# Optimization experiments

Measured on AMD Instinct MI355X. Metric: run time of the kernel, lower is better.

Reference implementation:

```python
import jax, jax.numpy as jnp
import numpy as np
from jax import lax

MAX_ALPHA = 0.00015
MAX_BETA = 0.00015
NOISE_GRAIN = 0.05
LN_EPS = 1e-5


def gaussian_blur(x, ksize, sigma):
    # depthwise 2D gaussian blur, same padding; x: [B, C, H, W]
    r = ksize // 2
    g = jnp.exp(-(jnp.linspace(-r, r, ksize, dtype=x.dtype) ** 2) / (2.0 * sigma ** 2))
    g = g / g.sum()
    k2d = g[:, None] * g[None, :]                       # [k, k]
    C = x.shape[1]
    kernel = jnp.broadcast_to(k2d, (C, 1, ksize, ksize))  # OIHW, depthwise
    return lax.conv_general_dilated(
        x, kernel, window_strides=(1, 1), padding=[(r, r), (r, r)],
        feature_group_count=C, dimension_numbers=('NCHW', 'OIHW', 'NCHW'))


def setup_inputs() -> dict:
    key = jax.random.key(0)
    ks = jax.random.split(key, 8)
    B, C, H, W = 8, 3, 1024, 1024
    L, D = 1024, 512
    Dh = D // 4
    return {
        'x_bg': jax.random.uniform(ks[0], (B, C, H, W), dtype=jnp.float32),
        'bottleneck_feat': jax.random.normal(ks[1], (B, L, D), dtype=jnp.float32),
        'mask': jax.random.uniform(ks[2], (B, 1, H, W), dtype=jnp.float32),
        'noise': jax.random.normal(ks[3], (B, C, H, W), dtype=jnp.float32),
        'W1': jax.random.normal(ks[4], (D, Dh), dtype=jnp.float32) * (1.0 / np.sqrt(D)),
        'b1': jnp.zeros((Dh,), dtype=jnp.float32),
        'ln_g': jnp.ones((Dh,), dtype=jnp.float32),
        'ln_b': jnp.zeros((Dh,), dtype=jnp.float32),
        'W2': jax.random.normal(ks[5], (Dh, 2), dtype=jnp.float32) * 0.01,
        'b2': jnp.zeros((2,), dtype=jnp.float32),
    }


def reference(x_bg, bottleneck_feat, mask, noise, W1, b1, ln_g, ln_b, W2, b2):
    # param head on global-pooled bottleneck feature
    feat_global = bottleneck_feat.mean(axis=1)                 # [B, D]
    h = feat_global @ W1 + b1                                  # [B, D/4]
    mu = h.mean(axis=-1, keepdims=True)
    var = ((h - mu) ** 2).mean(axis=-1, keepdims=True)
    h = (h - mu) * lax.rsqrt(var + LN_EPS) * ln_g + ln_b
    h = jax.nn.relu(h)
    params = h @ W2 + b2                                       # [B, 2]
    alpha = jax.nn.sigmoid(params[:, 0])[:, None, None, None] * MAX_ALPHA
    beta = jax.nn.sigmoid(params[:, 1])[:, None, None, None] * MAX_BETA

    # synthesize
    variance = alpha * x_bg + beta
    sigma = jnp.sqrt(jnp.maximum(variance, 1e-7))
    n = gaussian_blur(noise, 7, NOISE_GRAIN) * 1.5
    mask_soft = gaussian_blur(mask, 21, 5.0)                   # [B,1,H,W] broadcast
    noisy_output = x_bg + n * sigma * mask_soft
    return noisy_output, alpha, beta
```

## Files before the change

kernel.cpp:

```cpp
#include <hip/hip_runtime.h>
#include <math.h>

#define B 8
#define C 3
#define H 1024
#define W 1024
#define L 1024
#define D 512
#define DH 128
#define NPIX (H * W)
#define NOISY_ELEMS (B * C * NPIX)
#define TH 16

typedef float vf4 __attribute__((ext_vector_type(4)));

struct BlurW { float w[21]; };

__global__ void colsum_kernel(const float* __restrict__ feat, float* __restrict__ partial) {
    int blk = blockIdx.x;
    int b = blk >> 6, chunk = blk & 63;
    const float* base = feat + (size_t)b * (L * D) + (size_t)chunk * 16 * D;
    int t = threadIdx.x;
    float s0 = 0.f, s1 = 0.f;
    for (int l = 0; l < 16; ++l) {
        s0 += base[l * D + t];
        s1 += base[l * D + t + 256];
    }
    float* dst = partial + (size_t)blk * D;
    dst[t] = s0;
    dst[t + 256] = s1;
}

__global__ void head_kernel(const float* __restrict__ partial,
                            const float* __restrict__ W1, const float* __restrict__ b1,
                            const float* __restrict__ ln_g, const float* __restrict__ ln_b,
                            const float* __restrict__ W2, const float* __restrict__ b2,
                            float* __restrict__ ab, float* __restrict__ out_tail) {
    const int b = blockIdx.x;
    const int j = threadIdx.x;
    __shared__ float fm[D];
    __shared__ float red[DH];
    for (int d = j; d < D; d += DH) {
        float s = 0.f;
        const float* p = partial + (size_t)b * 64 * D + d;
        for (int c = 0; c < 64; ++c) s += p[c * D];
        fm[d] = s * (1.0f / (float)L);
    }
    __syncthreads();
    float h = b1[j];
    const vf4* fm4 = (const vf4*)fm;
    #pragma unroll 8
    for (int d4 = 0; d4 < D / 4; ++d4) {
        vf4 f = fm4[d4];
        h = fmaf(f.x, W1[(4 * d4 + 0) * DH + j], h);
        h = fmaf(f.y, W1[(4 * d4 + 1) * DH + j], h);
        h = fmaf(f.z, W1[(4 * d4 + 2) * DH + j], h);
        h = fmaf(f.w, W1[(4 * d4 + 3) * DH + j], h);
    }

    red[j] = h; __syncthreads();
    for (int s = 64; s > 0; s >>= 1) { if (j < s) red[j] += red[j + s]; __syncthreads(); }
    float mu = red[0] * (1.f / (float)DH);
    __syncthreads();
    float hc = h - mu;
    red[j] = hc * hc; __syncthreads();
    for (int s = 64; s > 0; s >>= 1) { if (j < s) red[j] += red[j + s]; __syncthreads(); }
    float var = red[0] * (1.f / (float)DH);
    __syncthreads();

    float hn = hc * rsqrtf(var + 1e-5f) * ln_g[j] + ln_b[j];
    hn = fmaxf(hn, 0.f);

    red[j] = hn * W2[j * 2 + 0]; __syncthreads();
    for (int s = 64; s > 0; s >>= 1) { if (j < s) red[j] += red[j + s]; __syncthreads(); }
    float p0 = red[0];
    __syncthreads();
    red[j] = hn * W2[j * 2 + 1]; __syncthreads();
    for (int s = 64; s > 0; s >>= 1) { if (j < s) red[j] += red[j + s]; __syncthreads(); }
    float p1 = red[0];

    if (j == 0) {
        float a  = 0.00015f / (1.f + expf(-(p0 + b2[0])));
        float be = 0.00015f / (1.f + expf(-(p1 + b2[1])));
        ab[b] = a; ab[8 + b] = be;
        out_tail[b] = a; out_tail[8 + b] = be;
    }
}

__global__ void hblur_kernel(const float* __restrict__ mask, float* __restrict__ hmask,
                             BlurW kw) {
    int row = blockIdx.x;
    const float* src = mask + (size_t)row * W;
    __shared__ float srow[W + 24];
    int t = threadIdx.x;
    if (t < 10) { srow[2 + t] = 0.f; srow[12 + W + t] = 0.f; }
    vf4 v = ((const vf4*)src)[t];
    ((vf4*)(srow + 12))[t] = v;
    __syncthreads();
    float* dst = hmask + (size_t)row * W;
    #pragma unroll
    for (int i = 0; i < 4; ++i) {
        int x = t + 256 * i;
        float acc = 0.f;
        #pragma unroll
        for (int k = 0; k < 21; ++k) acc = fmaf(kw.w[k], srow[x + 2 + k], acc);
        dst[x] = acc;
    }
}

__global__ __launch_bounds__(256) void final_kernel(
        const float* __restrict__ x_bg, const float* __restrict__ noise,
        const float* __restrict__ hmask, const float* __restrict__ ab,
        float* __restrict__ out, BlurW kw) {
    int blk = blockIdx.x;
    int b = blk >> 6;
    int s = blk & 63;
    int h0 = s * TH;
    int t = threadIdx.x;

    const vf4* hm4 = (const vf4*)hmask + (size_t)b * H * (W / 4) + t;
    const vf4 zero4 = {0.f, 0.f, 0.f, 0.f};

    vf4 win[21];
    #pragma unroll
    for (int k = 0; k < 21; ++k) {
        int hy = h0 - 10 + k;
        win[k] = (hy >= 0 && hy < H) ? hm4[(size_t)hy * (W / 4)] : zero4;
    }

    float alpha = ab[b], beta = ab[8 + b];
    const vf4* x4 = (const vf4*)x_bg;
    const vf4* n4 = (const vf4*)noise;
    vf4* o4 = (vf4*)out;

    #pragma unroll
    for (int r = 0; r < TH; ++r) {
        vf4 ms = zero4;
        #pragma unroll
        for (int k = 0; k < 21; ++k) {
            float wk = kw.w[k];
            vf4 v = win[(r + k) % 21];
            ms.x = fmaf(wk, v.x, ms.x);
            ms.y = fmaf(wk, v.y, ms.y);
            ms.z = fmaf(wk, v.z, ms.z);
            ms.w = fmaf(wk, v.w, ms.w);
        }
        int h = h0 + r;
        #pragma unroll
        for (int c = 0; c < C; ++c) {
            size_t idx = (((size_t)(b * C + c) * H) + h) * (W / 4) + t;
            vf4 x = __builtin_nontemporal_load(x4 + idx);
            vf4 nz = __builtin_nontemporal_load(n4 + idx);
            vf4 o;
            {
                float sg = sqrtf(fmaxf(fmaf(alpha, x.x, beta), 1e-7f));
                o.x = fmaf(1.5f * nz.x * sg, ms.x, x.x);
            }
            {
                float sg = sqrtf(fmaxf(fmaf(alpha, x.y, beta), 1e-7f));
                o.y = fmaf(1.5f * nz.y * sg, ms.y, x.y);
            }
            {
                float sg = sqrtf(fmaxf(fmaf(alpha, x.z, beta), 1e-7f));
                o.z = fmaf(1.5f * nz.z * sg, ms.z, x.z);
            }
            {
                float sg = sqrtf(fmaxf(fmaf(alpha, x.w, beta), 1e-7f));
                o.w = fmaf(1.5f * nz.w * sg, ms.w, x.w);
            }
            __builtin_nontemporal_store(o, o4 + idx);
        }
        if (r < TH - 1) {
            int hy = h0 + r + 11;
            win[r % 21] = (hy < H) ? hm4[(size_t)hy * (W / 4)] : zero4;
        }
    }
}

extern "C" void kernel_launch(void* const* d_in, const int* in_sizes, int n_in,
                              void* d_out, int out_size, void* d_ws, size_t ws_size,
                              hipStream_t stream) {
    const float* x_bg = (const float*)d_in[0];
    const float* feat = (const float*)d_in[1];
    const float* mask = (const float*)d_in[2];
    const float* noise = (const float*)d_in[3];
    const float* W1 = (const float*)d_in[4];
    const float* b1 = (const float*)d_in[5];
    const float* ln_g = (const float*)d_in[6];
    const float* ln_b = (const float*)d_in[7];
    const float* W2 = (const float*)d_in[8];
    const float* b2 = (const float*)d_in[9];
    float* out = (float*)d_out;

    float* ws_f = (float*)d_ws;
    float* partial = ws_f;
    float* ab = ws_f + 262144;
    float* hmask = ws_f + 262144 + 64;

    BlurW kw;
    {
        double g[21], s = 0.0;
        for (int i = 0; i < 21; ++i) { double x = (double)(i - 10); g[i] = exp(-x * x / 50.0); s += g[i]; }
        for (int i = 0; i < 21; ++i) kw.w[i] = (float)(g[i] / s);
    }

    colsum_kernel<<<B * 64, 256, 0, stream>>>(feat, partial);
    head_kernel<<<B, 128, 0, stream>>>(partial, W1, b1, ln_g, ln_b, W2, b2,
                                       ab, out + NOISY_ELEMS);
    hblur_kernel<<<B * H, 256, 0, stream>>>(mask, hmask, kw);
    final_kernel<<<B * (H / TH), 256, 0, stream>>>(x_bg, noise, hmask, ab, out, kw);
}
```

Before: 106.3 us.

## Fuse colsum into hblur launch, split final kernel per channel with XCD-aware block remap

Merges the feature column-sum and horizontal mask blur into one launch, so one kernel launch and its tail are removed. The final kernel now gives each channel its own workgroup, tripling the grid to raise parallelism. Both kernels remap block IDs so consecutive logical rows land on the same XCD, which should improve L2 locality for the shared hmask rows. In exchange, each channel block now recomputes the vertical 21-tap mask blur and reloads the mask window, tripling that work and its hmask reads.

```diff
diff --git a/kernel.cpp b/kernel.cpp
--- a/kernel.cpp
+++ b/kernel.cpp
@@ -16,19 +16,42 @@
 
 struct BlurW { float w[21]; };
 
-__global__ void colsum_kernel(const float* __restrict__ feat, float* __restrict__ partial) {
-    int blk = blockIdx.x;
-    int b = blk >> 6, chunk = blk & 63;
-    const float* base = feat + (size_t)b * (L * D) + (size_t)chunk * 16 * D;
+__global__ __launch_bounds__(256) void hblur_colsum_kernel(
+        const float* __restrict__ mask, float* __restrict__ hmask,
+        const float* __restrict__ feat, float* __restrict__ partial, BlurW kw) {
+    int wgid = blockIdx.x;
     int t = threadIdx.x;
-    float s0 = 0.f, s1 = 0.f;
-    for (int l = 0; l < 16; ++l) {
-        s0 += base[l * D + t];
-        s1 += base[l * D + t + 256];
-    }
-    float* dst = partial + (size_t)blk * D;
-    dst[t] = s0;
-    dst[t + 256] = s1;
+    __shared__ float srow[W + 24];
+
+    if (wgid < 8192) {
+        int l = (wgid & 7) * 1024 + (wgid >> 3);
+        const float* src = mask + (size_t)l * W;
+        if (t < 10) { srow[2 + t] = 0.f; srow[12 + W + t] = 0.f; }
+        vf4 v = __builtin_nontemporal_load((const vf4*)src + t);
+        ((vf4*)(srow + 12))[t] = v;
+        __syncthreads();
+        float* dst = hmask + (size_t)l * W;
+        #pragma unroll
+        for (int i = 0; i < 4; ++i) {
+            int x = t + 256 * i;
+            float acc = 0.f;
+            #pragma unroll
+            for (int k = 0; k < 21; ++k) acc = fmaf(kw.w[k], srow[x + 2 + k], acc);
+            dst[x] = acc;
+        }
+    } else {
+        int blk = wgid - 8192;
+        int b = blk >> 6, chunk = blk & 63;
+        const float* base = feat + (size_t)b * (L * D) + (size_t)chunk * 16 * D;
+        float s0 = 0.f, s1 = 0.f;
+        for (int ll = 0; ll < 16; ++ll) {
+            s0 += base[ll * D + t];
+            s1 += base[ll * D + t + 256];
+        }
+        float* dst = partial + (size_t)blk * D;
+        dst[t] = s0;
+        dst[t + 256] = s1;
+    }
 }
 
 __global__ void head_kernel(const float* __restrict__ partial,
@@ -87,34 +110,16 @@
     }
 }
 
-__global__ void hblur_kernel(const float* __restrict__ mask, float* __restrict__ hmask,
-                             BlurW kw) {
-    int row = blockIdx.x;
-    const float* src = mask + (size_t)row * W;
-    __shared__ float srow[W + 24];
-    int t = threadIdx.x;
-    if (t < 10) { srow[2 + t] = 0.f; srow[12 + W + t] = 0.f; }
-    vf4 v = ((const vf4*)src)[t];
-    ((vf4*)(srow + 12))[t] = v;
-    __syncthreads();
-    float* dst = hmask + (size_t)row * W;
-    #pragma unroll
-    for (int i = 0; i < 4; ++i) {
-        int x = t + 256 * i;
-        float acc = 0.f;
-        #pragma unroll
-        for (int k = 0; k < 21; ++k) acc = fmaf(kw.w[k], srow[x + 2 + k], acc);
-        dst[x] = acc;
-    }
-}
-
 __global__ __launch_bounds__(256) void final_kernel(
         const float* __restrict__ x_bg, const float* __restrict__ noise,
         const float* __restrict__ hmask, const float* __restrict__ ab,
         float* __restrict__ out, BlurW kw) {
-    int blk = blockIdx.x;
-    int b = blk >> 6;
-    int s = blk & 63;
+    int wgid = blockIdx.x;
+    int l = (wgid & 7) * 192 + (wgid >> 3);
+    int b = l / 192;
+    int rem = l - b * 192;
+    int s = rem / 3;
+    int c = rem - 3 * s;
     int h0 = s * TH;
     int t = threadIdx.x;
 
@@ -146,30 +151,27 @@
             ms.w = fmaf(wk, v.w, ms.w);
         }
         int h = h0 + r;
-        #pragma unroll
-        for (int c = 0; c < C; ++c) {
-            size_t idx = (((size_t)(b * C + c) * H) + h) * (W / 4) + t;
-            vf4 x = __builtin_nontemporal_load(x4 + idx);
-            vf4 nz = __builtin_nontemporal_load(n4 + idx);
-            vf4 o;
-            {
-                float sg = sqrtf(fmaxf(fmaf(alpha, x.x, beta), 1e-7f));
-                o.x = fmaf(1.5f * nz.x * sg, ms.x, x.x);
-            }
-            {
-                float sg = sqrtf(fmaxf(fmaf(alpha, x.y, beta), 1e-7f));
-                o.y = fmaf(1.5f * nz.y * sg, ms.y, x.y);
-            }
-            {
-                float sg = sqrtf(fmaxf(fmaf(alpha, x.z, beta), 1e-7f));
-                o.z = fmaf(1.5f * nz.z * sg, ms.z, x.z);
-            }
-            {
-                float sg = sqrtf(fmaxf(fmaf(alpha, x.w, beta), 1e-7f));
-                o.w = fmaf(1.5f * nz.w * sg, ms.w, x.w);
-            }
-            __builtin_nontemporal_store(o, o4 + idx);
-        }
+        size_t idx = (((size_t)(b * C + c) * H) + h) * (W / 4) + t;
+        vf4 x = __builtin_nontemporal_load(x4 + idx);
+        vf4 nz = __builtin_nontemporal_load(n4 + idx);
+        vf4 o;
+        {
+            float sg = sqrtf(fmaxf(fmaf(alpha, x.x, beta), 1e-7f));
+            o.x = fmaf(1.5f * nz.x * sg, ms.x, x.x);
+        }
+        {
+            float sg = sqrtf(fmaxf(fmaf(alpha, x.y, beta), 1e-7f));
+            o.y = fmaf(1.5f * nz.y * sg, ms.y, x.y);
+        }
+        {
+            float sg = sqrtf(fmaxf(fmaf(alpha, x.z, beta), 1e-7f));
+            o.z = fmaf(1.5f * nz.z * sg, ms.z, x.z);
+        }
+        {
+            float sg = sqrtf(fmaxf(fmaf(alpha, x.w, beta), 1e-7f));
+            o.w = fmaf(1.5f * nz.w * sg, ms.w, x.w);
+        }
+        __builtin_nontemporal_store(o, o4 + idx);
         if (r < TH - 1) {
             int hy = h0 + r + 11;
             win[r % 21] = (hy < H) ? hm4[(size_t)hy * (W / 4)] : zero4;
@@ -204,9 +206,8 @@
         for (int i = 0; i < 21; ++i) kw.w[i] = (float)(g[i] / s);
     }
 
-    colsum_kernel<<<B * 64, 256, 0, stream>>>(feat, partial);
+    hblur_colsum_kernel<<<8192 + 512, 256, 0, stream>>>(mask, hmask, feat, partial, kw);
     head_kernel<<<B, 128, 0, stream>>>(partial, W1, b1, ln_g, ln_b, W2, b2,
                                        ab, out + NOISY_ELEMS);
-    hblur_kernel<<<B * H, 256, 0, stream>>>(mask, hmask, kw);
-    final_kernel<<<B * (H / TH), 256, 0, stream>>>(x_bg, noise, hmask, ab, out, kw);
-}
+    final_kernel<<<B * (H / TH) * C, 256, 0, stream>>>(x_bg, noise, hmask, ab, out, kw);
+}
```

After: 112.0 us. 5.4% more time.
